# Kernel tuning notes

Hardware: AMD Instinct MI355X
Metric: run time of the kernel (lower is better)

## Reference

```python
import jax, jax.numpy as jnp
import numpy as np
from functools import partial

NUM_CLASSES = 6
IMG_H, IMG_W = 512, 512


def rasterize_boxes(bboxes, num_classes, hw):
    # bboxes: [B, num_organs, 4] int (xmin, ymin, xmax, ymax)
    H, W = hw
    bb = bboxes.astype(jnp.int32)
    xmin = jnp.clip(bb[..., 0], 0, W - 1)
    ymin = jnp.clip(bb[..., 1], 0, H - 1)
    xmax = jnp.maximum(xmin, jnp.minimum(bb[..., 2], W))
    ymax = jnp.maximum(ymin, jnp.minimum(bb[..., 3], H))
    rows = jnp.arange(H)[None, None, :, None]   # [1,1,H,1]
    cols = jnp.arange(W)[None, None, None, :]   # [1,1,1,W]
    mask = ((rows >= ymin[..., None, None]) & (rows < ymax[..., None, None]) &
            (cols >= xmin[..., None, None]) & (cols < xmax[..., None, None]))
    organs = mask.astype(jnp.float32)           # [B, num_organs, H, W]
    B = bboxes.shape[0]
    bg = jnp.zeros((B, 1, H, W), jnp.float32)   # channel 0 (background) stays 0
    return jnp.concatenate([bg, organs], axis=1)  # [B, num_classes, H, W]


def conv2d(x, w, stride=1, pad=0):
    return jax.lax.conv_general_dilated(
        x, w, window_strides=(stride, stride),
        padding=[(pad, pad), (pad, pad)],
        dimension_numbers=('NCHW', 'OIHW', 'NCHW'))


def bilinear_align_corners(x, out_h, out_w):
    # F.interpolate(..., mode='bilinear', align_corners=True)
    B, C, H, W = x.shape
    ys = jnp.linspace(0.0, H - 1.0, out_h)
    xs = jnp.linspace(0.0, W - 1.0, out_w)
    y0 = jnp.floor(ys).astype(jnp.int32); y1 = jnp.minimum(y0 + 1, H - 1)
    x0 = jnp.floor(xs).astype(jnp.int32); x1 = jnp.minimum(x0 + 1, W - 1)
    wy = (ys - y0).astype(x.dtype)[:, None]     # [out_h,1]
    wx = (xs - x0).astype(x.dtype)              # [out_w]
    top = x[:, :, y0, :]                        # [B,C,out_h,W]
    bot = x[:, :, y1, :]
    row = top * (1 - wy) + bot * wy             # [B,C,out_h,W]
    return row[..., x0] * (1 - wx) + row[..., x1] * wx


def sag(X_dec_c, X_dec_k, W_alpha, W_expand):
    attended = X_dec_c * X_dec_k
    alpha = jax.nn.softmax(conv2d(attended, W_alpha), axis=1)  # [B,num_classes,h,w]
    alpha_exp = conv2d(alpha, W_expand)                         # [B,C_sem,h,w]
    gated = jax.nn.sigmoid(X_dec_c * alpha_exp)
    return X_dec_c + gated


def setup_inputs() -> dict:
    key = jax.random.key(0)
    ks = jax.random.split(key, 6)
    B, C_sem, h, w = 4, 512, 32, 32
    num_organs = NUM_CLASSES - 1
    enc_final = jax.random.normal(ks[0], (B, C_sem, h, w), jnp.float32)
    bboxes = jax.random.randint(ks[1], (B, num_organs, 4), 0, IMG_W, jnp.int32)
    W_proc = jax.random.normal(ks[2], (C_sem, NUM_CLASSES, 3, 3), jnp.float32) * 0.1
    b_proc = jax.random.normal(ks[3], (C_sem,), jnp.float32) * 0.1
    W_alpha = jax.random.normal(ks[4], (NUM_CLASSES, C_sem, 1, 1), jnp.float32) * 0.05
    W_expand = jax.random.normal(ks[5], (C_sem, NUM_CLASSES, 1, 1), jnp.float32) * 0.05
    return {"enc_final": enc_final, "bboxes": bboxes, "W_proc": W_proc,
            "b_proc": b_proc, "W_alpha": W_alpha, "W_expand": W_expand}


def reference(enc_final, bboxes, W_proc, b_proc, W_alpha, W_expand):
    one_hot_map = rasterize_boxes(bboxes, NUM_CLASSES, (IMG_H, IMG_W))
    # Conv2d(num_classes -> enc_final_channels, k=3, s=2, p=1) + ReLU
    proc = jax.nn.relu(conv2d(one_hot_map, W_proc, stride=2, pad=1)
                       + b_proc[None, :, None, None])
    X_dec_k = bilinear_align_corners(proc, enc_final.shape[2], enc_final.shape[3])
    sag_out = sag(enc_final, X_dec_k, W_alpha, W_expand)
    return sag_out, one_hot_map, X_dec_k
```

## Files before the change

kernel.cpp:

```cpp
#include <hip/hip_runtime.h>
#include <math.h>

#define BATCH 4
#define CSEM 512
#define NORG 5
#define NCLS 6
#define HIMG 512
#define WIMG 512
#define HS 32
#define PH 256

#define SAG_N (BATCH*CSEM*HS*HS)
#define OH_N  (BATCH*NCLS*HIMG*WIMG)
#define OH_OFF SAG_N
#define XK_OFF (SAG_N + OH_N)
#define RASTER_BLOCKS (OH_N / 4 / 256)
#define SAG_BLOCKS    (BATCH * 32 * 4)

__global__ void k_xdeck_logits(const int* __restrict__ bb, const float* __restrict__ Wp,
                               const float* __restrict__ bp, const float* __restrict__ enc,
                               const float* __restrict__ Wa, float* __restrict__ xk,
                               float* __restrict__ part) {
    int blk = blockIdx.x;
    int cg = blk & 7;
    int oy = (blk >> 3) & 31;
    int b  = blk >> 8;
    int t  = threadIdx.x;
    int x  = t & 31;
    int c0 = t >> 5;

    float ysf = (float)(oy * 255.0 / 31.0);
    int y0 = (int)floorf(ysf);
    int y1 = min(y0 + 1, PH - 1);
    float wy = ysf - (float)y0;
    float xsf = (float)(x * 255.0 / 31.0);
    int x0 = (int)floorf(xsf);
    int x1 = min(x0 + 1, PH - 1);
    float wx = xsf - (float)x0;

    float ry0f[NORG][3], ry1f[NORG][3], cx0f[NORG][3], cx1f[NORG][3];
    bool act[NORG];
#pragma unroll
    for (int i = 0; i < NORG; i++) {
        const int* p = bb + (b * NORG + i) * 4;
        int xmin = min(max(p[0], 0), WIMG - 1);
        int ymin = min(max(p[1], 0), HIMG - 1);
        int xmax = max(xmin, min(p[2], WIMG));
        int ymax = max(ymin, min(p[3], HIMG));
        bool anyr = false, anyc = false;
#pragma unroll
        for (int k = 0; k < 3; k++) {
            int r0 = 2 * y0 - 1 + k, r1 = 2 * y1 - 1 + k;
            int cA = 2 * x0 - 1 + k, cB = 2 * x1 - 1 + k;
            float f0 = (r0 >= ymin && r0 < ymax) ? 1.f : 0.f;
            float f1 = (r1 >= ymin && r1 < ymax) ? 1.f : 0.f;
            float g0 = (cA >= xmin && cA < xmax) ? 1.f : 0.f;
            float g1 = (cB >= xmin && cB < xmax) ? 1.f : 0.f;
            ry0f[i][k] = f0; ry1f[i][k] = f1; cx0f[i][k] = g0; cx1f[i][k] = g1;
            anyr = anyr || (f0 > 0.f) || (f1 > 0.f);
            anyc = anyc || (g0 > 0.f) || (g1 > 0.f);
        }
        act[i] = anyr && anyc;
    }

    int cbase = cg * 64 + c0 * 8;
    float P[8][4];
#pragma unroll
    for (int cc = 0; cc < 8; cc++) {
        float bv = bp[cbase + cc];
        P[cc][0] = bv; P[cc][1] = bv; P[cc][2] = bv; P[cc][3] = bv;
    }

#pragma unroll
    for (int i = 0; i < NORG; i++) {
        if (!act[i]) continue;
        float c00 = cx0f[i][0], c01 = cx0f[i][1], c02 = cx0f[i][2];
        float c10 = cx1f[i][0], c11 = cx1f[i][1], c12 = cx1f[i][2];
        float r00 = ry0f[i][0], r01 = ry0f[i][1], r02 = ry0f[i][2];
        float r10 = ry1f[i][0], r11 = ry1f[i][1], r12 = ry1f[i][2];
#pragma unroll
        for (int cc = 0; cc < 8; cc++) {
            const float* w = Wp + (size_t)((cbase + cc) * NCLS + i + 1) * 9;
            float w0 = w[0], w1 = w[1], w2 = w[2];
            float w3 = w[3], w4 = w[4], w5 = w[5];
            float w6 = w[6], w7 = w[7], w8 = w[8];
            float s00 = w0 * c00 + w1 * c01 + w2 * c02;
            float s01 = w3 * c00 + w4 * c01 + w5 * c02;
            float s02 = w6 * c00 + w7 * c01 + w8 * c02;
            float s10 = w0 * c10 + w1 * c11 + w2 * c12;
            float s11 = w3 * c10 + w4 * c11 + w5 * c12;
            float s12 = w6 * c10 + w7 * c11 + w8 * c12;
            P[cc][0] += s00 * r00 + s01 * r01 + s02 * r02;
            P[cc][1] += s10 * r00 + s11 * r01 + s12 * r02;
            P[cc][2] += s00 * r10 + s01 * r11 + s02 * r12;
            P[cc][3] += s10 * r10 + s11 * r11 + s12 * r12;
        }
    }

    float acc[NCLS] = {0, 0, 0, 0, 0, 0};
#pragma unroll
    for (int cc = 0; cc < 8; cc++) {
        int c = cbase + cc;
        float p00 = fmaxf(P[cc][0], 0.f);
        float p01 = fmaxf(P[cc][1], 0.f);
        float p10 = fmaxf(P[cc][2], 0.f);
        float p11 = fmaxf(P[cc][3], 0.f);
        float t0 = p00 * (1.f - wy) + p10 * wy;
        float t1 = p01 * (1.f - wy) + p11 * wy;
        float val = t0 * (1.f - wx) + t1 * wx;
        int idx = ((b * CSEM + c) * HS + oy) * HS + x;
        xk[idx] = val;
        float att = enc[idx] * val;
#pragma unroll
        for (int o = 0; o < NCLS; o++) acc[o] += Wa[o * CSEM + c] * att;
    }

    __shared__ float red[NCLS][8][32];
#pragma unroll
    for (int o = 0; o < NCLS; o++) red[o][c0][x] = acc[o];
    __syncthreads();
    if (t < NCLS * 32) {
        int o = t >> 5;
        int xx = t & 31;
        float s = 0.f;
#pragma unroll
        for (int j = 0; j < 8; j++) s += red[o][j][xx];
        part[(((cg * BATCH + b) * NCLS + o) * HS + oy) * HS + xx] = s;
    }
}

__global__ void k_sag_raster(const float* __restrict__ part, const float* __restrict__ enc,
                             const float* __restrict__ We, const int* __restrict__ bb,
                             float* __restrict__ out, float* __restrict__ oh) {
    int blk = blockIdx.x;
    int t = threadIdx.x;

    if (blk < RASTER_BLOCKS) {
        int idx = blk * 256 + t;
        int x4 = (idx & 127) << 2;
        int tt = idx >> 7;
        int y  = tt & 511;
        int bc = tt >> 9;
        int ch = bc % NCLS;
        int b  = bc / NCLS;
        float4 v = make_float4(0.f, 0.f, 0.f, 0.f);
        if (ch != 0) {
            const int* p = bb + (b * NORG + (ch - 1)) * 4;
            int xmin = min(max(p[0], 0), WIMG - 1);
            int ymin = min(max(p[1], 0), HIMG - 1);
            int xmax = max(xmin, min(p[2], WIMG));
            int ymax = max(ymin, min(p[3], HIMG));
            if (y >= ymin && y < ymax) {
                v.x = (x4 + 0 >= xmin && x4 + 0 < xmax) ? 1.f : 0.f;
                v.y = (x4 + 1 >= xmin && x4 + 1 < xmax) ? 1.f : 0.f;
                v.z = (x4 + 2 >= xmin && x4 + 2 < xmax) ? 1.f : 0.f;
                v.w = (x4 + 3 >= xmin && x4 + 3 < xmax) ? 1.f : 0.f;
            }
        }
        reinterpret_cast<float4*>(oh)[idx] = v;
        return;
    }

    blk -= RASTER_BLOCKS;
    int sl = blk & 3;
    int oy = (blk >> 2) & 31;
    int b  = blk >> 7;

    __shared__ float lg[NCLS][32];
    if (t < NCLS * 32) {
        int o = t >> 5;
        int x = t & 31;
        float s = 0.f;
#pragma unroll
        for (int cg = 0; cg < 8; cg++)
            s += part[(((cg * BATCH + b) * NCLS + o) * HS + oy) * HS + x];
        lg[o][x] = s;
    }
    __syncthreads();
    if (t < 32) {
        float l[NCLS];
#pragma unroll
        for (int o = 0; o < NCLS; o++) l[o] = lg[o][t];
        float m = l[0];
#pragma unroll
        for (int o = 1; o < NCLS; o++) m = fmaxf(m, l[o]);
        float sum = 0.f;
#pragma unroll
        for (int o = 0; o < NCLS; o++) { l[o] = expf(l[o] - m); sum += l[o]; }
        float inv = 1.f / sum;
#pragma unroll
        for (int o = 0; o < NCLS; o++) lg[o][t] = l[o] * inv;
    }
    __syncthreads();

    int x4 = (t & 7) << 2;
    int cq = t >> 3;
#pragma unroll
    for (int j = 0; j < 4; j++) {
        int c = sl * 128 + cq * 4 + j;
        int idx4 = (((b * CSEM + c) * HS + oy) * HS + x4) >> 2;
        float4 e = reinterpret_cast<const float4*>(enc)[idx4];
        float4 ae = make_float4(0.f, 0.f, 0.f, 0.f);
#pragma unroll
        for (int o = 0; o < NCLS; o++) {
            float w = We[c * NCLS + o];
            ae.x += w * lg[o][x4 + 0];
            ae.y += w * lg[o][x4 + 1];
            ae.z += w * lg[o][x4 + 2];
            ae.w += w * lg[o][x4 + 3];
        }
        float4 r;
        r.x = e.x + 1.f / (1.f + expf(-e.x * ae.x));
        r.y = e.y + 1.f / (1.f + expf(-e.y * ae.y));
        r.z = e.z + 1.f / (1.f + expf(-e.z * ae.z));
        r.w = e.w + 1.f / (1.f + expf(-e.w * ae.w));
        reinterpret_cast<float4*>(out)[idx4] = r;
    }
}

extern "C" void kernel_launch(void* const* d_in, const int* in_sizes, int n_in,
                              void* d_out, int out_size, void* d_ws, size_t ws_size,
                              hipStream_t stream) {
    const float* enc = (const float*)d_in[0];
    const int*   bb  = (const int*)d_in[1];
    const float* Wp  = (const float*)d_in[2];
    const float* bp  = (const float*)d_in[3];
    const float* Wa  = (const float*)d_in[4];
    const float* We  = (const float*)d_in[5];
    float* out = (float*)d_out;
    float* sag = out;
    float* oh  = out + OH_OFF;
    float* xk  = out + XK_OFF;
    float* part = (float*)d_ws;

    k_xdeck_logits<<<BATCH * 32 * 8, 256, 0, stream>>>(bb, Wp, bp, enc, Wa, xk, part);
    k_sag_raster  <<<RASTER_BLOCKS + SAG_BLOCKS, 256, 0, stream>>>(part, enc, We, bb, sag, oh);
}
```

Measured before the change: 94.10 us.

## Move rasterization into first kernel and split SAG stage across more blocks

The one-hot rasterization blocks move from the second kernel into the first, where they run alongside the X_dec_k/logit blocks, so the second kernel holds only the softmax and SAG gating. The SAG stage now uses 1024 blocks that each handle 64 channels instead of 512 blocks that each handle 128. This is meant to overlap the large raster write with the compute-heavy conv blocks and to leave a short, well-parallelized tail kernel. In exchange, each SAG block recomputes the softmax over the partial logits, which doubles that redundant work.

```diff
diff --git a/kernel.cpp b/kernel.cpp
--- a/kernel.cpp
+++ b/kernel.cpp
@@ -14,129 +14,18 @@
 #define OH_N  (BATCH*NCLS*HIMG*WIMG)
 #define OH_OFF SAG_N
 #define XK_OFF (SAG_N + OH_N)
+#define XDECK_BLOCKS  (BATCH * 32 * 8)
 #define RASTER_BLOCKS (OH_N / 4 / 256)
-#define SAG_BLOCKS    (BATCH * 32 * 4)
-
-__global__ void k_xdeck_logits(const int* __restrict__ bb, const float* __restrict__ Wp,
+
+__global__ void k_xdeck_raster(const int* __restrict__ bb, const float* __restrict__ Wp,
                                const float* __restrict__ bp, const float* __restrict__ enc,
                                const float* __restrict__ Wa, float* __restrict__ xk,
-                               float* __restrict__ part) {
-    int blk = blockIdx.x;
-    int cg = blk & 7;
-    int oy = (blk >> 3) & 31;
-    int b  = blk >> 8;
-    int t  = threadIdx.x;
-    int x  = t & 31;
-    int c0 = t >> 5;
-
-    float ysf = (float)(oy * 255.0 / 31.0);
-    int y0 = (int)floorf(ysf);
-    int y1 = min(y0 + 1, PH - 1);
-    float wy = ysf - (float)y0;
-    float xsf = (float)(x * 255.0 / 31.0);
-    int x0 = (int)floorf(xsf);
-    int x1 = min(x0 + 1, PH - 1);
-    float wx = xsf - (float)x0;
-
-    float ry0f[NORG][3], ry1f[NORG][3], cx0f[NORG][3], cx1f[NORG][3];
-    bool act[NORG];
-#pragma unroll
-    for (int i = 0; i < NORG; i++) {
-        const int* p = bb + (b * NORG + i) * 4;
-        int xmin = min(max(p[0], 0), WIMG - 1);
-        int ymin = min(max(p[1], 0), HIMG - 1);
-        int xmax = max(xmin, min(p[2], WIMG));
-        int ymax = max(ymin, min(p[3], HIMG));
-        bool anyr = false, anyc = false;
-#pragma unroll
-        for (int k = 0; k < 3; k++) {
-            int r0 = 2 * y0 - 1 + k, r1 = 2 * y1 - 1 + k;
-            int cA = 2 * x0 - 1 + k, cB = 2 * x1 - 1 + k;
-            float f0 = (r0 >= ymin && r0 < ymax) ? 1.f : 0.f;
-            float f1 = (r1 >= ymin && r1 < ymax) ? 1.f : 0.f;
-            float g0 = (cA >= xmin && cA < xmax) ? 1.f : 0.f;
-            float g1 = (cB >= xmin && cB < xmax) ? 1.f : 0.f;
-            ry0f[i][k] = f0; ry1f[i][k] = f1; cx0f[i][k] = g0; cx1f[i][k] = g1;
-            anyr = anyr || (f0 > 0.f) || (f1 > 0.f);
-            anyc = anyc || (g0 > 0.f) || (g1 > 0.f);
-        }
-        act[i] = anyr && anyc;
-    }
-
-    int cbase = cg * 64 + c0 * 8;
-    float P[8][4];
-#pragma unroll
-    for (int cc = 0; cc < 8; cc++) {
-        float bv = bp[cbase + cc];
-        P[cc][0] = bv; P[cc][1] = bv; P[cc][2] = bv; P[cc][3] = bv;
-    }
-
-#pragma unroll
-    for (int i = 0; i < NORG; i++) {
-        if (!act[i]) continue;
-        float c00 = cx0f[i][0], c01 = cx0f[i][1], c02 = cx0f[i][2];
-        float c10 = cx1f[i][0], c11 = cx1f[i][1], c12 = cx1f[i][2];
-        float r00 = ry0f[i][0], r01 = ry0f[i][1], r02 = ry0f[i][2];
-        float r10 = ry1f[i][0], r11 = ry1f[i][1], r12 = ry1f[i][2];
-#pragma unroll
-        for (int cc = 0; cc < 8; cc++) {
-            const float* w = Wp + (size_t)((cbase + cc) * NCLS + i + 1) * 9;
-            float w0 = w[0], w1 = w[1], w2 = w[2];
-            float w3 = w[3], w4 = w[4], w5 = w[5];
-            float w6 = w[6], w7 = w[7], w8 = w[8];
-            float s00 = w0 * c00 + w1 * c01 + w2 * c02;
-            float s01 = w3 * c00 + w4 * c01 + w5 * c02;
-            float s02 = w6 * c00 + w7 * c01 + w8 * c02;
-            float s10 = w0 * c10 + w1 * c11 + w2 * c12;
-            float s11 = w3 * c10 + w4 * c11 + w5 * c12;
-            float s12 = w6 * c10 + w7 * c11 + w8 * c12;
-            P[cc][0] += s00 * r00 + s01 * r01 + s02 * r02;
-            P[cc][1] += s10 * r00 + s11 * r01 + s12 * r02;
-            P[cc][2] += s00 * r10 + s01 * r11 + s02 * r12;
-            P[cc][3] += s10 * r10 + s11 * r11 + s12 * r12;
-        }
-    }
-
-    float acc[NCLS] = {0, 0, 0, 0, 0, 0};
-#pragma unroll
-    for (int cc = 0; cc < 8; cc++) {
-        int c = cbase + cc;
-        float p00 = fmaxf(P[cc][0], 0.f);
-        float p01 = fmaxf(P[cc][1], 0.f);
-        float p10 = fmaxf(P[cc][2], 0.f);
-        float p11 = fmaxf(P[cc][3], 0.f);
-        float t0 = p00 * (1.f - wy) + p10 * wy;
-        float t1 = p01 * (1.f - wy) + p11 * wy;
-        float val = t0 * (1.f - wx) + t1 * wx;
-        int idx = ((b * CSEM + c) * HS + oy) * HS + x;
-        xk[idx] = val;
-        float att = enc[idx] * val;
-#pragma unroll
-        for (int o = 0; o < NCLS; o++) acc[o] += Wa[o * CSEM + c] * att;
-    }
-
-    __shared__ float red[NCLS][8][32];
-#pragma unroll
-    for (int o = 0; o < NCLS; o++) red[o][c0][x] = acc[o];
-    __syncthreads();
-    if (t < NCLS * 32) {
-        int o = t >> 5;
-        int xx = t & 31;
-        float s = 0.f;
-#pragma unroll
-        for (int j = 0; j < 8; j++) s += red[o][j][xx];
-        part[(((cg * BATCH + b) * NCLS + o) * HS + oy) * HS + xx] = s;
-    }
-}
-
-__global__ void k_sag_raster(const float* __restrict__ part, const float* __restrict__ enc,
-                             const float* __restrict__ We, const int* __restrict__ bb,
-                             float* __restrict__ out, float* __restrict__ oh) {
+                               float* __restrict__ part, float* __restrict__ oh) {
     int blk = blockIdx.x;
     int t = threadIdx.x;
 
-    if (blk < RASTER_BLOCKS) {
-        int idx = blk * 256 + t;
+    if (blk >= XDECK_BLOCKS) {
+        int idx = (blk - XDECK_BLOCKS) * 256 + t;
         int x4 = (idx & 127) << 2;
         int tt = idx >> 7;
         int y  = tt & 511;
@@ -161,10 +50,119 @@
         return;
     }
 
-    blk -= RASTER_BLOCKS;
-    int sl = blk & 3;
-    int oy = (blk >> 2) & 31;
-    int b  = blk >> 7;
+    int cg = blk & 7;
+    int oy = (blk >> 3) & 31;
+    int b  = blk >> 8;
+    int x  = t & 31;
+    int c0 = t >> 5;
+
+    float ysf = (float)(oy * 255.0 / 31.0);
+    int y0 = (int)floorf(ysf);
+    int y1 = min(y0 + 1, PH - 1);
+    float wy = ysf - (float)y0;
+    float xsf = (float)(x * 255.0 / 31.0);
+    int x0 = (int)floorf(xsf);
+    int x1 = min(x0 + 1, PH - 1);
+    float wx = xsf - (float)x0;
+
+    float ry0f[NORG][3], ry1f[NORG][3], cx0f[NORG][3], cx1f[NORG][3];
+    bool act[NORG];
+#pragma unroll
+    for (int i = 0; i < NORG; i++) {
+        const int* p = bb + (b * NORG + i) * 4;
+        int xmin = min(max(p[0], 0), WIMG - 1);
+        int ymin = min(max(p[1], 0), HIMG - 1);
+        int xmax = max(xmin, min(p[2], WIMG));
+        int ymax = max(ymin, min(p[3], HIMG));
+        bool anyr = false, anyc = false;
+#pragma unroll
+        for (int k = 0; k < 3; k++) {
+            int r0 = 2 * y0 - 1 + k, r1 = 2 * y1 - 1 + k;
+            int cA = 2 * x0 - 1 + k, cB = 2 * x1 - 1 + k;
+            float f0 = (r0 >= ymin && r0 < ymax) ? 1.f : 0.f;
+            float f1 = (r1 >= ymin && r1 < ymax) ? 1.f : 0.f;
+            float g0 = (cA >= xmin && cA < xmax) ? 1.f : 0.f;
+            float g1 = (cB >= xmin && cB < xmax) ? 1.f : 0.f;
+            ry0f[i][k] = f0; ry1f[i][k] = f1; cx0f[i][k] = g0; cx1f[i][k] = g1;
+            anyr = anyr || (f0 > 0.f) || (f1 > 0.f);
+            anyc = anyc || (g0 > 0.f) || (g1 > 0.f);
+        }
+        act[i] = anyr && anyc;
+    }
+
+    int cbase = cg * 64 + c0 * 8;
+    float P[8][4];
+#pragma unroll
+    for (int cc = 0; cc < 8; cc++) {
+        float bv = bp[cbase + cc];
+        P[cc][0] = bv; P[cc][1] = bv; P[cc][2] = bv; P[cc][3] = bv;
+    }
+
+#pragma unroll
+    for (int i = 0; i < NORG; i++) {
+        if (!act[i]) continue;
+        float c00 = cx0f[i][0], c01 = cx0f[i][1], c02 = cx0f[i][2];
+        float c10 = cx1f[i][0], c11 = cx1f[i][1], c12 = cx1f[i][2];
+        float r00 = ry0f[i][0], r01 = ry0f[i][1], r02 = ry0f[i][2];
+        float r10 = ry1f[i][0], r11 = ry1f[i][1], r12 = ry1f[i][2];
+#pragma unroll
+        for (int cc = 0; cc < 8; cc++) {
+            const float* w = Wp + (size_t)((cbase + cc) * NCLS + i + 1) * 9;
+            float w0 = w[0], w1 = w[1], w2 = w[2];
+            float w3 = w[3], w4 = w[4], w5 = w[5];
+            float w6 = w[6], w7 = w[7], w8 = w[8];
+            float s00 = w0 * c00 + w1 * c01 + w2 * c02;
+            float s01 = w3 * c00 + w4 * c01 + w5 * c02;
+            float s02 = w6 * c00 + w7 * c01 + w8 * c02;
+            float s10 = w0 * c10 + w1 * c11 + w2 * c12;
+            float s11 = w3 * c10 + w4 * c11 + w5 * c12;
+            float s12 = w6 * c10 + w7 * c11 + w8 * c12;
+            P[cc][0] += s00 * r00 + s01 * r01 + s02 * r02;
+            P[cc][1] += s10 * r00 + s11 * r01 + s12 * r02;
+            P[cc][2] += s00 * r10 + s01 * r11 + s02 * r12;
+            P[cc][3] += s10 * r10 + s11 * r11 + s12 * r12;
+        }
+    }
+
+    float acc[NCLS] = {0, 0, 0, 0, 0, 0};
+#pragma unroll
+    for (int cc = 0; cc < 8; cc++) {
+        int c = cbase + cc;
+        float p00 = fmaxf(P[cc][0], 0.f);
+        float p01 = fmaxf(P[cc][1], 0.f);
+        float p10 = fmaxf(P[cc][2], 0.f);
+        float p11 = fmaxf(P[cc][3], 0.f);
+        float t0 = p00 * (1.f - wy) + p10 * wy;
+        float t1 = p01 * (1.f - wy) + p11 * wy;
+        float val = t0 * (1.f - wx) + t1 * wx;
+        int idx = ((b * CSEM + c) * HS + oy) * HS + x;
+        xk[idx] = val;
+        float att = enc[idx] * val;
+#pragma unroll
+        for (int o = 0; o < NCLS; o++) acc[o] += Wa[o * CSEM + c] * att;
+    }
+
+    __shared__ float red[NCLS][8][32];
+#pragma unroll
+    for (int o = 0; o < NCLS; o++) red[o][c0][x] = acc[o];
+    __syncthreads();
+    if (t < NCLS * 32) {
+        int o = t >> 5;
+        int xx = t & 31;
+        float s = 0.f;
+#pragma unroll
+        for (int j = 0; j < 8; j++) s += red[o][j][xx];
+        part[(((cg * BATCH + b) * NCLS + o) * HS + oy) * HS + xx] = s;
+    }
+}
+
+__global__ void k_softmax_sag(const float* __restrict__ part, const float* __restrict__ enc,
+                              const float* __restrict__ We, float* __restrict__ out) {
+    int blk = blockIdx.x;
+    int cg = blk & 7;
+    int oy = (blk >> 3) & 31;
+    int b  = blk >> 8;
+    int t  = threadIdx.x;
 
     __shared__ float lg[NCLS][32];
     if (t < NCLS * 32) {
@@ -172,8 +170,8 @@
         int x = t & 31;
         float s = 0.f;
 #pragma unroll
-        for (int cg = 0; cg < 8; cg++)
-            s += part[(((cg * BATCH + b) * NCLS + o) * HS + oy) * HS + x];
+        for (int g = 0; g < 8; g++)
+            s += part[(((g * BATCH + b) * NCLS + o) * HS + oy) * HS + x];
         lg[o][x] = s;
     }
     __syncthreads();
@@ -194,10 +192,10 @@
     __syncthreads();
 
     int x4 = (t & 7) << 2;
-    int cq = t >> 3;
-#pragma unroll
-    for (int j = 0; j < 4; j++) {
-        int c = sl * 128 + cq * 4 + j;
+    int cc = t >> 3;
+#pragma unroll
+    for (int j = 0; j < 2; j++) {
+        int c = cg * 64 + cc * 2 + j;
         int idx4 = (((b * CSEM + c) * HS + oy) * HS + x4) >> 2;
         float4 e = reinterpret_cast<const float4*>(enc)[idx4];
         float4 ae = make_float4(0.f, 0.f, 0.f, 0.f);
@@ -233,6 +231,7 @@
     float* xk  = out + XK_OFF;
     float* part = (float*)d_ws;
 
-    k_xdeck_logits<<<BATCH * 32 * 8, 256, 0, stream>>>(bb, Wp, bp, enc, Wa, xk, part);
-    k_sag_raster  <<<RASTER_BLOCKS + SAG_BLOCKS, 256, 0, stream>>>(part, enc, We, bb, sag, oh);
+    k_xdeck_raster<<<XDECK_BLOCKS + RASTER_BLOCKS, 256, 0, stream>>>(
+        bb, Wp, bp, enc, Wa, xk, part, oh);
+    k_softmax_sag <<<XDECK_BLOCKS, 256, 0, stream>>>(part, enc, We, sag);
 }
```

Result: faster. 89.84 us (-4.5%).
